# Optimization experiments

Hardware: AMD Instinct MI355X
Metric: run time of the kernel (lower is better)

Reference implementation:

```python
import jax, jax.numpy as jnp
import numpy as np

B, C, L = 8, 512, 512
MAX_LEN = 48
LAST_WIN = 64  # hard-coded final window in the torch module


def _fofe_all(x, alpha, max_len):
    """Windowed FOFE encoder.

    Torch semantics: out[:, :, i, t] = sum_{k=0}^{w_i-1} alpha^k * x[:, :, t-1-k]
    (zero outside [0, L-1]), for windows w_i = 0..max_len-1 plus w=64,
    produced there by per-window depthwise conv1d with left pad w.
    We compute it via the linear recurrence z[t] = alpha*z[t-1] + x[t]
    (associative scan) and the windowed identity
    out_w[t] = z[t-1] - alpha^w * z[t-1-w].
    """
    Bx, Cx, Lx = x.shape
    # per-channel decay broadcast over (B, C, L)
    a = jnp.broadcast_to(alpha[None, :, 0:1], x.shape)

    def comb(c1, c2):
        a1, b1 = c1
        a2, b2 = c2
        return (a1 * a2, a2 * b1 + b2)

    _, z = jax.lax.associative_scan(comb, (a, x), axis=-1)  # z[t] = sum_k alpha^k x[t-k]

    windows_i = jnp.concatenate([jnp.arange(max_len), jnp.array([LAST_WIN])])  # (nw,)
    windows_f = windows_i.astype(x.dtype)
    W = max(max_len - 1, LAST_WIN)  # largest left shift needed
    zp = jnp.pad(z, ((0, 0), (0, 0), (W + 1, 0)))  # zeros for negative time indices

    t = jnp.arange(Lx + 1)
    base = zp[:, :, W + t]  # z[t-1], shape (B, C, L+1)
    idx = t[None, :] + (W - windows_i[:, None])  # (nw, L+1), all >= 0
    shifted = zp[:, :, idx]  # z[t-1-w], shape (B, C, nw, L+1)
    ap = jnp.power(alpha, windows_f[None, :])  # (C, nw); alpha is (C,1)
    out = base[:, :, None, :] - ap[None, :, :, None] * shifted  # (B, C, nw, L+1)
    return out


def setup_inputs() -> dict:
    key = jax.random.key(0)
    kx, = jax.random.split(key, 1)
    x = jax.random.normal(kx, (B, C, L), dtype=jnp.float32)
    alpha = jnp.full((C, 1), 0.8, dtype=jnp.float32)  # learned per-channel decay, init 0.8
    return {"x": x, "alpha": alpha, "max_len": MAX_LEN}


def reference(x, alpha, max_len):
    return _fofe_all(x, alpha, max_len)
```

## Files before the change

### kernel.cpp

```cpp
#include <hip/hip_runtime.h>


#define CC 512
#define LL 512
#define NW 49
#define LO 513
#define SLAB (NW * LO)
#define GRID 256
#define NTAU 16
#define ZOFF 65
#define ZROW 640

typedef float f32x4 __attribute__((ext_vector_type(4)));

__device__ __forceinline__ int swz(int i) { return i ^ ((i >> 5) & 3); }

__global__ __launch_bounds__(512)
void fofe_kernel(const float* __restrict__ x,
                 const float* __restrict__ alpha,
                 float* __restrict__ out)
{
    __shared__ float zs[NTAU][ZROW];

    const int tid  = threadIdx.x;
    const int wid  = tid >> 6;
    const int lane = tid & 63;
    const int blk  = blockIdx.x;

    for (int tau = wid; tau < NTAU; tau += 8) {
        const int g = tau * GRID + blk;
        const float al = alpha[g & (CC - 1)];
        const float* xr = x + (size_t)g * LL;

        const f32x4 xv0 = reinterpret_cast<const f32x4*>(xr)[lane * 2];
        const f32x4 xv1 = reinterpret_cast<const f32x4*>(xr)[lane * 2 + 1];
        const float xe[8] = {xv0.x, xv0.y, xv0.z, xv0.w,
                             xv1.x, xv1.y, xv1.z, xv1.w};
        float l[8];
        {
            float s = 0.f;
            #pragma unroll
            for (int m = 0; m < 8; ++m) { s = fmaf(al, s, xe[m]); l[m] = s; }
        }
        float pw[8];
        {
            float p = al;
            #pragma unroll
            for (int m = 0; m < 8; ++m) { pw[m] = p; p *= al; }
        }
        float A = pw[7], S = l[7];
        #pragma unroll
        for (int off = 1; off < 64; off <<= 1) {
            const float Ap = __shfl_up(A, off);
            const float Sp = __shfl_up(S, off);
            if (lane >= off) { S = fmaf(A, Sp, S); A = A * Ap; }
        }
        float carry = __shfl_up(S, 1);
        if (lane == 0) carry = 0.f;

        float* z = zs[tau];
        z[swz(lane)] = 0.f;
        if (lane == 0) z[swz(64)] = 0.f;
        #pragma unroll
        for (int m = 0; m < 8; ++m)
            z[swz(ZOFF + lane * 8 + m)] = fmaf(pw[m], carry, l[m]);
    }
    __syncthreads();

    for (int tau = 0; tau < NTAU; ++tau) {
        const int g = tau * GRID + blk;
        const float al = alpha[g & (CC - 1)];
        const float* z = zs[tau];
        float* oslab = out + (size_t)g * SLAB;

        const float a2  = al * al, a4 = a2 * a2, a8 = a4 * a4;
        const float a16 = a8 * a8;
        const float a64 = (a16 * a16) * (a16 * a16);

        float p = 1.f;
        {
            float m = al;
            #pragma unroll
            for (int b = 0; b < 3; ++b) { if (wid & (1 << b)) p *= m; m *= m; }
        }

        for (int i = wid; i < NW; i += 8) {
            const int   w   = (i < 48) ? i : 64;
            const float apw = (i < 48) ? p : a64;
            float* op = oslab + i * LO;
            const int q    = (g + i) & 3;
            const int peel = (4 - q) & 3;
            const int k0b  = ZOFF - 1;

            if (lane < peel)
                op[lane] = fmaf(-apw, z[swz(k0b + lane - w)], z[swz(k0b + lane)]);

            const int nf4  = (LO - peel) >> 2;
            const int tail = (LO - peel) & 3;
            for (int f = lane; f < nf4; f += 64) {
                const int t0 = peel + 4 * f;
                const int k0 = k0b + t0;
                f32x4 v;
                v.x = fmaf(-apw, z[swz(k0     - w)], z[swz(k0    )]);
                v.y = fmaf(-apw, z[swz(k0 + 1 - w)], z[swz(k0 + 1)]);
                v.z = fmaf(-apw, z[swz(k0 + 2 - w)], z[swz(k0 + 2)]);
                v.w = fmaf(-apw, z[swz(k0 + 3 - w)], z[swz(k0 + 3)]);
                *reinterpret_cast<f32x4*>(op + t0) = v;
            }
            if (lane < tail) {
                const int t = peel + 4 * nf4 + lane;
                op[t] = fmaf(-apw, z[swz(k0b + t - w)], z[swz(k0b + t)]);
            }
            p *= a8;
        }
        __syncthreads();
    }
}

extern "C" void kernel_launch(void* const* d_in, const int* in_sizes, int n_in,
                              void* d_out, int out_size, void* d_ws, size_t ws_size,
                              hipStream_t stream)
{
    const float* x     = (const float*)d_in[0];
    const float* alpha = (const float*)d_in[1];
    float* out = (float*)d_out;

    fofe_kernel<<<GRID, 512, 0, stream>>>(x, alpha, out);
}
```

Before: 85.90 us.

## Flatten per-channel output slab into one contiguous vectorized store loop with power LUT

Instead of each wave writing one window row of 513 floats with per-row peel and tail handling, all 512 threads now sweep the whole contiguous 49x513 slab with 16-byte aligned stores, so there is only one peel and one tail per channel. Per-window decay powers are precomputed into a shared-memory table before the sync, so each element looks up its coefficient. The change aims to cut the idle lanes and partial-wave work caused by 513-wide rows split across only 8 waves. In exchange each vector needs an integer divide by 513 to find its row, and vectors that straddle a row boundary fall back to a scalar path.

```diff
diff --git a/kernel.cpp b/kernel.cpp
--- a/kernel.cpp
+++ b/kernel.cpp
@@ -21,6 +21,7 @@
                  float* __restrict__ out)
 {
     __shared__ float zs[NTAU][ZROW];
+    __shared__ float lut[NTAU][NW];
 
     const int tid  = threadIdx.x;
     const int wid  = tid >> 6;
@@ -65,53 +66,62 @@
         for (int m = 0; m < 8; ++m)
             z[swz(ZOFF + lane * 8 + m)] = fmaf(pw[m], carry, l[m]);
     }
+    if (tid < NW) {
+        const int w = (tid < 48) ? tid : 64;
+        for (int tau = 0; tau < NTAU; ++tau) {
+            const int g = tau * GRID + blk;
+            const float al = alpha[g & (CC - 1)];
+            float p = 1.f, m = al;
+            #pragma unroll
+            for (int b = 0; b < 7; ++b) { if (w & (1 << b)) p *= m; m *= m; }
+            lut[tau][tid] = p;
+        }
+    }
     __syncthreads();
 
     for (int tau = 0; tau < NTAU; ++tau) {
         const int g = tau * GRID + blk;
-        const float al = alpha[g & (CC - 1)];
-        const float* z = zs[tau];
+        const float* z  = zs[tau];
+        const float* lu = lut[tau];
         float* oslab = out + (size_t)g * SLAB;
 
-        const float a2  = al * al, a4 = a2 * a2, a8 = a4 * a4;
-        const float a16 = a8 * a8;
-        const float a64 = (a16 * a16) * (a16 * a16);
+        auto eval1 = [&](int e) -> float {
+            const unsigned i = (unsigned)e / 513u;
+            const int t = e - (int)i * 513;
+            const int w = (i < 48u) ? (int)i : 64;
+            return fmaf(-lu[i], z[swz(ZOFF - 1 + t - w)], z[swz(ZOFF - 1 + t)]);
+        };
 
-        float p = 1.f;
-        {
-            float m = al;
-            #pragma unroll
-            for (int b = 0; b < 3; ++b) { if (wid & (1 << b)) p *= m; m *= m; }
-        }
+        const int peel  = (4 - (g & 3)) & 3;
+        const int nf4   = (SLAB - peel) >> 2;
+        const int ntail = (SLAB - peel) & 3;
 
-        for (int i = wid; i < NW; i += 8) {
-            const int   w   = (i < 48) ? i : 64;
-            const float apw = (i < 48) ? p : a64;
-            float* op = oslab + i * LO;
-            const int q    = (g + i) & 3;
-            const int peel = (4 - q) & 3;
-            const int k0b  = ZOFF - 1;
+        if (tid < peel)  oslab[tid] = eval1(tid);
+        if (tid < ntail) oslab[peel + 4 * nf4 + tid] = eval1(peel + 4 * nf4 + tid);
 
-            if (lane < peel)
-                op[lane] = fmaf(-apw, z[swz(k0b + lane - w)], z[swz(k0b + lane)]);
+        for (int f = tid; f < nf4; f += 512) {
+            const int e = peel + 4 * f;
+            const unsigned i = (unsigned)e / 513u;
+            const int t = e - (int)i * 513;
 
-            const int nf4  = (LO - peel) >> 2;
-            const int tail = (LO - peel) & 3;
-            for (int f = lane; f < nf4; f += 64) {
-                const int t0 = peel + 4 * f;
-                const int k0 = k0b + t0;
+            if (t <= 509) {
+                const int   w   = (i < 48u) ? (int)i : 64;
+                const float apw = lu[i];
+                const int   k0  = ZOFF - 1 + t;
                 f32x4 v;
                 v.x = fmaf(-apw, z[swz(k0     - w)], z[swz(k0    )]);
                 v.y = fmaf(-apw, z[swz(k0 + 1 - w)], z[swz(k0 + 1)]);
                 v.z = fmaf(-apw, z[swz(k0 + 2 - w)], z[swz(k0 + 2)]);
                 v.w = fmaf(-apw, z[swz(k0 + 3 - w)], z[swz(k0 + 3)]);
-                *reinterpret_cast<f32x4*>(op + t0) = v;
+                *reinterpret_cast<f32x4*>(oslab + e) = v;
+            } else {
+                f32x4 v;
+                v.x = eval1(e);
+                v.y = eval1(e + 1);
+                v.z = eval1(e + 2);
+                v.w = eval1(e + 3);
+                *reinterpret_cast<f32x4*>(oslab + e) = v;
             }
-            if (lane < tail) {
-                const int t = peel + 4 * nf4 + lane;
-                op[t] = fmaf(-apw, z[swz(k0b + t - w)], z[swz(k0b + t)]);
-            }
-            p *= a8;
         }
         __syncthreads();
     }
```

New measurement: 100.3 us. +16.7%, slower.

## Compute successive windows by incremental recurrence over staged x and drop per-row syncs

Applied to the files above, without the earlier changes.

Stages the raw x row in shared memory next to the prefix z. Each wave pair now owns 12 consecutive windows over half the time axis, with 4 outputs per lane. Each window is derived from the previous one with out_{w+1}[t] = out_w[t] + alpha^w x[t-1-w], replacing two z lookups per output. The w=64 window and the middle column t=256 are handled separately, the latter by a wave-level scan, and the per-channel __syncthreads is removed. In exchange, 16-byte stores are no longer alignment-peeled, rounding error builds up along the recurrence, and the kernel stays bound by output write bandwidth.

```diff
diff --git a/kernel.cpp b/kernel.cpp
--- a/kernel.cpp
+++ b/kernel.cpp
@@ -10,6 +10,8 @@
 #define NTAU 16
 #define ZOFF 65
 #define ZROW 640
+#define XPAD 48
+#define XROW 560
 
 typedef float f32x4 __attribute__((ext_vector_type(4)));
 
@@ -21,6 +23,7 @@
                  float* __restrict__ out)
 {
     __shared__ float zs[NTAU][ZROW];
+    __shared__ float xs[NTAU][XROW];
 
     const int tid  = threadIdx.x;
     const int wid  = tid >> 6;
@@ -58,62 +61,95 @@
         float carry = __shfl_up(S, 1);
         if (lane == 0) carry = 0.f;
 
-        float* z = zs[tau];
+        float* z  = zs[tau];
+        float* xw = xs[tau];
         z[swz(lane)] = 0.f;
         if (lane == 0) z[swz(64)] = 0.f;
+        if (lane < XPAD) xw[swz(lane)] = 0.f;
         #pragma unroll
-        for (int m = 0; m < 8; ++m)
+        for (int m = 0; m < 8; ++m) {
             z[swz(ZOFF + lane * 8 + m)] = fmaf(pw[m], carry, l[m]);
+            xw[swz(XPAD + lane * 8 + m)] = xe[m];
+        }
     }
     __syncthreads();
+
+    const int rg   = wid >> 1;
+    const int half = wid & 1;
+    const int t0   = half * 257 + 4 * lane;
+    const int j0   = 12 * rg;
 
     for (int tau = 0; tau < NTAU; ++tau) {
         const int g = tau * GRID + blk;
         const float al = alpha[g & (CC - 1)];
-        const float* z = zs[tau];
+        const float* z  = zs[tau];
+        const float* xw = xs[tau];
         float* oslab = out + (size_t)g * SLAB;
-
-        const float a2  = al * al, a4 = a2 * a2, a8 = a4 * a4;
-        const float a16 = a8 * a8;
-        const float a64 = (a16 * a16) * (a16 * a16);
 
         float p = 1.f;
         {
             float m = al;
             #pragma unroll
-            for (int b = 0; b < 3; ++b) { if (wid & (1 << b)) p *= m; m *= m; }
+            for (int b = 0; b < 6; ++b) { if (j0 & (1 << b)) p *= m; m *= m; }
         }
 
-        for (int i = wid; i < NW; i += 8) {
-            const int   w   = (i < 48) ? i : 64;
-            const float apw = (i < 48) ? p : a64;
-            float* op = oslab + i * LO;
-            const int q    = (g + i) & 3;
-            const int peel = (4 - q) & 3;
-            const int k0b  = ZOFF - 1;
+        const int kb = ZOFF - 1 + t0;
+        f32x4 acc;
+        acc.x = fmaf(-p, z[swz(kb     - j0)], z[swz(kb    )]);
+        acc.y = fmaf(-p, z[swz(kb + 1 - j0)], z[swz(kb + 1)]);
+        acc.z = fmaf(-p, z[swz(kb + 2 - j0)], z[swz(kb + 2)]);
+        acc.w = fmaf(-p, z[swz(kb + 3 - j0)], z[swz(kb + 3)]);
 
-            if (lane < peel)
-                op[lane] = fmaf(-apw, z[swz(k0b + lane - w)], z[swz(k0b + lane)]);
+        const int xb = XPAD + t0 - 1 - j0;
+        float w0 = xw[swz(xb)];
+        float w1 = xw[swz(xb + 1)];
+        float w2 = xw[swz(xb + 2)];
+        float w3 = xw[swz(xb + 3)];
 
-            const int nf4  = (LO - peel) >> 2;
-            const int tail = (LO - peel) & 3;
-            for (int f = lane; f < nf4; f += 64) {
-                const int t0 = peel + 4 * f;
-                const int k0 = k0b + t0;
-                f32x4 v;
-                v.x = fmaf(-apw, z[swz(k0     - w)], z[swz(k0    )]);
-                v.y = fmaf(-apw, z[swz(k0 + 1 - w)], z[swz(k0 + 1)]);
-                v.z = fmaf(-apw, z[swz(k0 + 2 - w)], z[swz(k0 + 2)]);
-                v.w = fmaf(-apw, z[swz(k0 + 3 - w)], z[swz(k0 + 3)]);
-                *reinterpret_cast<f32x4*>(op + t0) = v;
+        float* op = oslab + j0 * LO + t0;
+        #pragma unroll
+        for (int s = 0; s < 12; ++s) {
+            f32x4 tv = acc;
+            __builtin_memcpy(op, &tv, 16);
+            op += LO;
+            if (s < 11) {
+                const float nw = xw[swz(xb - 1 - s)];
+                acc.x = fmaf(p, w0, acc.x);
+                acc.y = fmaf(p, w1, acc.y);
+                acc.z = fmaf(p, w2, acc.z);
+                acc.w = fmaf(p, w3, acc.w);
+                w3 = w2; w2 = w1; w1 = w0; w0 = nw;
+                p *= al;
             }
-            if (lane < tail) {
-                const int t = peel + 4 * nf4 + lane;
-                op[t] = fmaf(-apw, z[swz(k0b + t - w)], z[swz(k0b + t)]);
+        }
+
+        if (rg == 1) {
+            float a64 = al;
+            #pragma unroll
+            for (int b = 0; b < 6; ++b) a64 *= a64;
+            f32x4 v;
+            v.x = fmaf(-a64, z[swz(kb     - 64)], z[swz(kb    )]);
+            v.y = fmaf(-a64, z[swz(kb + 1 - 64)], z[swz(kb + 1)]);
+            v.z = fmaf(-a64, z[swz(kb + 2 - 64)], z[swz(kb + 2)]);
+            v.w = fmaf(-a64, z[swz(kb + 3 - 64)], z[swz(kb + 3)]);
+            __builtin_memcpy(oslab + 48 * LO + t0, &v, 16);
+        }
+
+        if (wid == 0) {
+            float pl = 1.f, mm = al;
+            #pragma unroll
+            for (int b = 0; b < 6; ++b) { if (lane & (1 << b)) pl *= mm; mm *= mm; }
+            float s = pl * xw[swz(XPAD + 255 - lane)];
+            #pragma unroll
+            for (int off = 1; off < 64; off <<= 1) {
+                const float v = __shfl_up(s, off);
+                if (lane >= off) s += v;
             }
-            p *= a8;
+            float* ocol = oslab + 256;
+            if (lane <= 46) ocol[(lane + 1) * LO] = s;
+            if (lane == 47) ocol[0] = 0.f;
+            if (lane == 63) ocol[48 * LO] = s;
         }
-        __syncthreads();
     }
 }
 
```

After: 107.0 us. 1.25x slower.
